# Kernel optimization log

Measured on AMD Instinct MI355X. Metric: run time of the kernel, lower is better.

## Reference

```python
import jax, jax.numpy as jnp
import numpy as np
from jax import lax

B, IMG, P, STRIDE, CIN = 4, 256, 8, 8, 1
D, NH, L = 768, 8, 21
GRID = (IMG - P) // STRIDE + 1  # 32
N = GRID * GRID                 # 1024 tokens
HD = D // NH                    # 96
SCALE = float(HD) ** -0.5


def setup_inputs() -> dict:
    key = jax.random.key(0)
    ks = jax.random.split(key, 9)
    s = 0.02
    return {
        "sam": jax.random.normal(ks[0], (B, CIN, IMG, IMG), dtype=jnp.float32),
        "conv_w": jax.random.normal(ks[1], (D, CIN, P, P), dtype=jnp.float32) * s,
        "conv_b": jnp.zeros((D,), dtype=jnp.float32),
        "ln_g": jnp.ones((D,), dtype=jnp.float32),
        "ln_b": jnp.zeros((D,), dtype=jnp.float32),
        "pos": jax.random.normal(ks[2], (N, D), dtype=jnp.float32) * s,
        "q_w": jax.random.normal(ks[3], (L, D, D), dtype=jnp.float32) * s,
        "kv_w": jax.random.normal(ks[4], (L, D, 2 * D), dtype=jnp.float32) * s,
        "proj_w": jax.random.normal(ks[5], (L, D, D), dtype=jnp.float32) * s,
        "proj_b": jnp.zeros((L, D), dtype=jnp.float32),
    }


def _layernorm(x, g, b, eps=1e-5):
    mu = jnp.mean(x, axis=-1, keepdims=True)
    var = jnp.mean(jnp.square(x - mu), axis=-1, keepdims=True)
    return (x - mu) * lax.rsqrt(var + eps) * g + b


def _guidance(x, qw, kvw, pw, pb):
    b, n, c = x.shape
    q = jnp.einsum('bnc,cd->bnd', x, qw).reshape(b, n, NH, HD).transpose(0, 2, 1, 3)
    kv = jnp.einsum('bnc,cd->bnd', x, kvw)
    k = kv[..., :c].reshape(b, n, NH, HD).transpose(0, 2, 1, 3)
    v = kv[..., c:].reshape(b, n, NH, HD).transpose(0, 2, 1, 3)
    attn = jax.nn.softmax(jnp.einsum('bhnd,bhmd->bhnm', q, k) * SCALE, axis=-1)
    o = jnp.einsum('bhnm,bhmd->bhnd', attn, v).transpose(0, 2, 1, 3).reshape(b, n, c)
    o = jnp.einsum('bnc,cd->bnd', o, pw) + pb
    return o + x  # residual (dropouts are identity in eval)


def reference(sam, conv_w, conv_b, ln_g, ln_b, pos, q_w, kv_w, proj_w, proj_b):
    # Patch embed: conv (valid, stride=patch) -> [B,D,32,32] -> tokens -> LN
    y = lax.conv_general_dilated(sam, conv_w, window_strides=(STRIDE, STRIDE),
                                 padding='VALID',
                                 dimension_numbers=('NCHW', 'OIHW', 'NCHW'))
    y = y + conv_b[None, :, None, None]
    y = y.reshape(B, D, N).transpose(0, 2, 1)  # [B,N,D]
    y = _layernorm(y, ln_g, ln_b)
    x0 = y + pos[None]  # pos_embed(arange) broadcast over batch
    # Faithful to source: each block consumes the SAME x0; output is last block's.
    out = x0
    for i in range(L):
        out = _guidance(x0, q_w[i], kv_w[i], proj_w[i], proj_b[i])
    return out
```

## Files before the change

kernel.cpp:

```cpp
#include <hip/hip_runtime.h>
#include <hip/hip_bf16.h>

typedef __attribute__((ext_vector_type(4))) float f32x4;
typedef __attribute__((ext_vector_type(8))) short s16x8;
typedef unsigned short u16;
typedef unsigned int u32;

#define DEV __device__ __forceinline__

DEV u16 f2bf(float f) {
  union { float f; u32 u; } v; v.f = f;
  u32 r = v.u + 0x7fffu + ((v.u >> 16) & 1u);
  return (u16)(r >> 16);
}

#define MFMA16(a, b, c) __builtin_amdgcn_mfma_f32_16x16x32_bf16((a), (b), (c), 0, 0, 0)
#define GLD16(g, l) __builtin_amdgcn_global_load_lds((const __attribute__((address_space(1))) u32*)(g), (__attribute__((address_space(3))) u32*)(l), 16, 0, 0)

__global__ __launch_bounds__(256) void wcvt_k(const float* __restrict__ src,
                                              u16* __restrict__ dst,
                                              int ncols, float scale) {
  __shared__ float tb[32][33];
  int tile = blockIdx.x;
  int tk = (tile % 24) * 32;
  int tn = (tile / 24) * 32;
  int tx = threadIdx.x & 31, ty = threadIdx.x >> 5;
#pragma unroll
  for (int i = 0; i < 4; i++)
    tb[ty + i * 8][tx] = src[(size_t)(tk + ty + i * 8) * ncols + tn + tx];
  __syncthreads();
#pragma unroll
  for (int i = 0; i < 4; i++)
    dst[(size_t)(tn + ty + i * 8) * 768 + tk + tx] = f2bf(tb[tx][ty + i * 8] * scale);
}

__global__ __launch_bounds__(256) void patch_ln(
    const float* __restrict__ sam, const float* __restrict__ cw,
    const float* __restrict__ cb, const float* __restrict__ g,
    const float* __restrict__ bb, const float* __restrict__ pos,
    float* __restrict__ x0f, u16* __restrict__ x0b) {
  int blk = blockIdx.x;
  int b = blk >> 8, nq = blk & 255;
  int t = threadIdx.x;
  __shared__ float pix[4][64];
  {
    int tk = t >> 6, p = t & 63;
    int n = nq * 4 + tk;
    int gi = n >> 5, gj = n & 31;
    pix[tk][p] = sam[b * 65536 + (gi * 8 + (p >> 3)) * 256 + gj * 8 + (p & 7)];
  }
  __syncthreads();
  float acc[3][4];
#pragma unroll
  for (int u = 0; u < 3; u++) {
    int d = t + u * 256;
    const float4* w4 = (const float4*)(cw + (size_t)d * 64);
    float a0 = cb[d];
    float av0 = a0, av1 = a0, av2 = a0, av3 = a0;
#pragma unroll
    for (int pc = 0; pc < 16; pc++) {
      float4 w = w4[pc];
      av0 += w.x * pix[0][pc * 4] + w.y * pix[0][pc * 4 + 1] + w.z * pix[0][pc * 4 + 2] + w.w * pix[0][pc * 4 + 3];
      av1 += w.x * pix[1][pc * 4] + w.y * pix[1][pc * 4 + 1] + w.z * pix[1][pc * 4 + 2] + w.w * pix[1][pc * 4 + 3];
      av2 += w.x * pix[2][pc * 4] + w.y * pix[2][pc * 4 + 1] + w.z * pix[2][pc * 4 + 2] + w.w * pix[2][pc * 4 + 3];
      av3 += w.x * pix[3][pc * 4] + w.y * pix[3][pc * 4 + 1] + w.z * pix[3][pc * 4 + 2] + w.w * pix[3][pc * 4 + 3];
    }
    acc[u][0] = av0; acc[u][1] = av1; acc[u][2] = av2; acc[u][3] = av3;
  }
  float s1[4], s2[4];
#pragma unroll
  for (int tk = 0; tk < 4; tk++) {
    s1[tk] = acc[0][tk] + acc[1][tk] + acc[2][tk];
    s2[tk] = acc[0][tk] * acc[0][tk] + acc[1][tk] * acc[1][tk] + acc[2][tk] * acc[2][tk];
  }
#pragma unroll
  for (int m = 1; m < 64; m <<= 1) {
#pragma unroll
    for (int tk = 0; tk < 4; tk++) {
      s1[tk] += __shfl_xor(s1[tk], m);
      s2[tk] += __shfl_xor(s2[tk], m);
    }
  }
  __shared__ float red[2][4][4];
  int wid = t >> 6;
  if ((t & 63) == 0) {
#pragma unroll
    for (int tk = 0; tk < 4; tk++) { red[0][wid][tk] = s1[tk]; red[1][wid][tk] = s2[tk]; }
  }
  __syncthreads();
  float mu[4], rs[4];
#pragma unroll
  for (int tk = 0; tk < 4; tk++) {
    float S1 = red[0][0][tk] + red[0][1][tk] + red[0][2][tk] + red[0][3][tk];
    float S2 = red[1][0][tk] + red[1][1][tk] + red[1][2][tk] + red[1][3][tk];
    mu[tk] = S1 * (1.0f / 768.0f);
    float var = S2 * (1.0f / 768.0f) - mu[tk] * mu[tk];
    rs[tk] = rsqrtf(var + 1e-5f);
  }
#pragma unroll
  for (int u = 0; u < 3; u++) {
    int d = t + u * 256;
    float gg = g[d], bbv = bb[d];
#pragma unroll
    for (int tk = 0; tk < 4; tk++) {
      int n = nq * 4 + tk;
      float val = (acc[u][tk] - mu[tk]) * rs[tk] * gg + bbv + pos[(size_t)n * 768 + d];
      size_t idx = ((size_t)(b * 1024 + n)) * 768 + d;
      x0f[idx] = val;
      x0b[idx] = f2bf(val);
    }
  }
}

template <int EPI>
__global__ __launch_bounds__(256, 2) void gemm128(
    const u16* __restrict__ A, const u16* __restrict__ BT, int M, int N, int K,
    u16* __restrict__ q, u16* __restrict__ kk_, u16* __restrict__ vt,
    const float* __restrict__ pb, const float* __restrict__ x0f,
    float* __restrict__ outp) {
  __shared__ __align__(16) u16 Al[128 * 32];
  __shared__ __align__(16) u16 Bl[128 * 32];
  int m0 = blockIdx.y * 128, n0 = blockIdx.x * 128;
  int tid = threadIdx.x, lane = tid & 63, wid = tid >> 6;
  int wr = wid >> 1, wc = wid & 1;
  f32x4 acc[4][4] = {};
  int arow = lane >> 2, acol = (lane & 3) * 8;
  const u16* ag = A + (size_t)(m0 + wid * 32 + arow) * K + acol;
  const u16* bg = BT + (size_t)(n0 + wid * 32 + arow) * K + acol;
  u16* alp = Al + wid * 32 * 32;
  u16* blp = Bl + wid * 32 * 32;
  for (int kt = 0; kt < K; kt += 32) {
    GLD16(ag + kt, alp);
    GLD16(ag + kt + 16 * K, alp + 16 * 32);
    GLD16(bg + kt, blp);
    GLD16(bg + kt + 16 * K, blp + 16 * 32);
    __syncthreads();
    s16x8 af[4], bf[4];
#pragma unroll
    for (int m = 0; m < 4; m++)
      af[m] = *(const s16x8*)&Al[(wr * 64 + m * 16 + (lane & 15)) * 32 + (lane >> 4) * 8];
#pragma unroll
    for (int nn = 0; nn < 4; nn++)
      bf[nn] = *(const s16x8*)&Bl[(wc * 64 + nn * 16 + (lane & 15)) * 32 + (lane >> 4) * 8];
#pragma unroll
    for (int m = 0; m < 4; m++)
#pragma unroll
      for (int nn = 0; nn < 4; nn++)
        acc[m][nn] = MFMA16(af[m], bf[nn], acc[m][nn]);
    __syncthreads();
  }
#pragma unroll
  for (int m = 0; m < 4; m++) {
    int rbase = m0 + wr * 64 + m * 16 + ((lane >> 4) << 2);
#pragma unroll
    for (int nn = 0; nn < 4; nn++) {
      int col = n0 + wc * 64 + nn * 16 + (lane & 15);
      f32x4 v = acc[m][nn];
      if (EPI == 0) {
        if (col < 1536) {
          int cc = (col < 768) ? col : col - 768;
          int h = cc / 96, hd = cc % 96;
          u16* dst = (col < 768) ? q : kk_;
          int bq = (rbase >> 10) * 8 + h;
#pragma unroll
          for (int i = 0; i < 4; i++) {
            int row = rbase + i;
            dst[((size_t)bq * 1024 + (row & 1023)) * 96 + hd] = f2bf(v[i]);
          }
        } else {
          int cc = col - 1536;
          int h = cc / 96, hd = cc % 96;
          int bq = (rbase >> 10) * 8 + h;
          ushort4 pk;
          pk.x = f2bf(v[0]); pk.y = f2bf(v[1]); pk.z = f2bf(v[2]); pk.w = f2bf(v[3]);
          *(ushort4*)&vt[((size_t)bq * 96 + hd) * 1024 + (rbase & 1023)] = pk;
        }
      } else {
        float add = pb[col];
#pragma unroll
        for (int i = 0; i < 4; i++) {
          size_t idx = (size_t)(rbase + i) * 768 + col;
          outp[idx] = v[i] + add + x0f[idx];
        }
      }
    }
  }
}

__global__ __launch_bounds__(256, 2) void attn_k(
    const u16* __restrict__ qg, const u16* __restrict__ kg,
    const u16* __restrict__ vg, u16* __restrict__ o) {
  int bh = blockIdx.x >> 3, qb = blockIdx.x & 7;
  int b = bh >> 3, h = bh & 7;
  int tid = threadIdx.x, lane = tid & 63, wid = tid >> 6;
  int q0 = qb * 128 + wid * 32;
  s16x8 aq[2][3];
#pragma unroll
  for (int mf = 0; mf < 2; mf++)
#pragma unroll
    for (int kc = 0; kc < 3; kc++)
      aq[mf][kc] = *(const s16x8*)&qg[((size_t)bh * 1024 + q0 + mf * 16 + (lane & 15)) * 96 + kc * 32 + (lane >> 4) * 8];
  float mrun[2][4], lrun[2][4];
  f32x4 accO[2][6] = {};
#pragma unroll
  for (int mf = 0; mf < 2; mf++)
#pragma unroll
    for (int i = 0; i < 4; i++) { mrun[mf][i] = -1e30f; lrun[mf][i] = 0.0f; }
  __shared__ __align__(16) u16 Kl[64][104];
  __shared__ __align__(16) u16 VTl[96][72];
  __shared__ __align__(16) u16 Pl[4][32][72];
  const u16* kbase = kg + (size_t)bh * 1024 * 96;
  const u16* vbase = vg + (size_t)bh * 96 * 1024;
  int kkey[3], koff[3], vhd[3], vko[3];
#pragma unroll
  for (int it = 0; it < 3; it++) {
    int c = it * 256 + tid;
    kkey[it] = c / 12; koff[it] = (c % 12) * 8;
    vhd[it] = c >> 3;  vko[it] = (c & 7) * 8;
  }
  for (int kt = 0; kt < 16; kt++) {
#pragma unroll
    for (int it = 0; it < 3; it++) {
      *(uint4*)&Kl[kkey[it]][koff[it]] = *(const uint4*)&kbase[(size_t)(kt * 64 + kkey[it]) * 96 + koff[it]];
      *(uint4*)&VTl[vhd[it]][vko[it]] = *(const uint4*)&vbase[(size_t)vhd[it] * 1024 + kt * 64 + vko[it]];
    }
    __syncthreads();
    f32x4 s[2][4] = {};
#pragma unroll
    for (int nf = 0; nf < 4; nf++) {
#pragma unroll
      for (int kc = 0; kc < 3; kc++) {
        s16x8 bk = *(const s16x8*)&Kl[nf * 16 + (lane & 15)][kc * 32 + (lane >> 4) * 8];
        s[0][nf] = MFMA16(aq[0][kc], bk, s[0][nf]);
        s[1][nf] = MFMA16(aq[1][kc], bk, s[1][nf]);
      }
    }
#pragma unroll
    for (int mf = 0; mf < 2; mf++) {
#pragma unroll
      for (int i = 0; i < 4; i++) {
        float rm = fmaxf(fmaxf(s[mf][0][i], s[mf][1][i]), fmaxf(s[mf][2][i], s[mf][3][i]));
#pragma unroll
        for (int m = 1; m < 16; m <<= 1) rm = fmaxf(rm, __shfl_xor(rm, m));
        float newm = fmaxf(mrun[mf][i], rm);
        float alpha = __expf(mrun[mf][i] - newm);
        float ps = 0.0f;
#pragma unroll
        for (int nf = 0; nf < 4; nf++) {
          float p = __expf(s[mf][nf][i] - newm);
          s[mf][nf][i] = p;
          ps += p;
        }
#pragma unroll
        for (int m = 1; m < 16; m <<= 1) ps += __shfl_xor(ps, m);
        lrun[mf][i] = lrun[mf][i] * alpha + ps;
        mrun[mf][i] = newm;
#pragma unroll
        for (int nf = 0; nf < 6; nf++) accO[mf][nf][i] *= alpha;
      }
#pragma unroll
      for (int nf = 0; nf < 4; nf++)
#pragma unroll
        for (int i = 0; i < 4; i++)
          Pl[wid][mf * 16 + ((lane >> 4) << 2) + i][nf * 16 + (lane & 15)] = f2bf(s[mf][nf][i]);
    }
    asm volatile("s_waitcnt lgkmcnt(0)" ::: "memory");
    __builtin_amdgcn_sched_barrier(0);
#pragma unroll
    for (int kc = 0; kc < 2; kc++) {
      s16x8 ap0 = *(const s16x8*)&Pl[wid][0 + (lane & 15)][kc * 32 + (lane >> 4) * 8];
      s16x8 ap1 = *(const s16x8*)&Pl[wid][16 + (lane & 15)][kc * 32 + (lane >> 4) * 8];
#pragma unroll
      for (int nf = 0; nf < 6; nf++) {
        s16x8 bv = *(const s16x8*)&VTl[nf * 16 + (lane & 15)][kc * 32 + (lane >> 4) * 8];
        accO[0][nf] = MFMA16(ap0, bv, accO[0][nf]);
        accO[1][nf] = MFMA16(ap1, bv, accO[1][nf]);
      }
    }
    __syncthreads();
  }
#pragma unroll
  for (int mf = 0; mf < 2; mf++) {
#pragma unroll
    for (int i = 0; i < 4; i++) {
      float inv = 1.0f / lrun[mf][i];
      int tok = qb * 128 + wid * 32 + mf * 16 + ((lane >> 4) << 2) + i;
      u16* orow = o + ((size_t)(b * 1024 + tok)) * 768 + h * 96;
#pragma unroll
      for (int nf = 0; nf < 6; nf++)
        orow[nf * 16 + (lane & 15)] = f2bf(accO[mf][nf][i] * inv);
    }
  }
}

extern "C" void kernel_launch(void* const* d_in, const int* in_sizes, int n_in,
                              void* d_out, int out_size, void* d_ws, size_t ws_size,
                              hipStream_t stream) {
  const float* sam    = (const float*)d_in[0];
  const float* conv_w = (const float*)d_in[1];
  const float* conv_b = (const float*)d_in[2];
  const float* ln_g   = (const float*)d_in[3];
  const float* ln_b   = (const float*)d_in[4];
  const float* pos    = (const float*)d_in[5];
  const float* q_w    = (const float*)d_in[6] + (size_t)20 * 768 * 768;
  const float* kv_w   = (const float*)d_in[7] + (size_t)20 * 768 * 1536;
  const float* proj_w = (const float*)d_in[8] + (size_t)20 * 768 * 768;
  const float* proj_b = (const float*)d_in[9] + (size_t)20 * 768;

  char* ws = (char*)d_ws;
  float* x0f  = (float*)ws; ws += (size_t)4096 * 768 * 4;
  u16* x0b    = (u16*)ws;   ws += (size_t)4096 * 768 * 2;
  u16* wqkvT  = (u16*)ws;   ws += (size_t)2304 * 768 * 2;
  u16* pwT    = (u16*)ws;   ws += (size_t)768 * 768 * 2;
  u16* qs     = (u16*)ws;   ws += (size_t)32 * 1024 * 96 * 2;
  u16* ks     = (u16*)ws;   ws += (size_t)32 * 1024 * 96 * 2;
  u16* vts    = (u16*)ws;   ws += (size_t)32 * 96 * 1024 * 2;
  u16* ob     = (u16*)ws;   ws += (size_t)4096 * 768 * 2;

  const float SCALE = 0.10206207261596577f;

  wcvt_k<<<24 * 24, 256, 0, stream>>>(q_w, wqkvT, 768, SCALE);
  wcvt_k<<<24 * 48, 256, 0, stream>>>(kv_w, wqkvT + (size_t)768 * 768, 1536, 1.0f);
  wcvt_k<<<24 * 24, 256, 0, stream>>>(proj_w, pwT, 768, 1.0f);
  patch_ln<<<1024, 256, 0, stream>>>(sam, conv_w, conv_b, ln_g, ln_b, pos, x0f, x0b);
  dim3 g1(18, 32);
  gemm128<0><<<g1, 256, 0, stream>>>(x0b, wqkvT, 4096, 2304, 768, qs, ks, vts,
                                     nullptr, nullptr, nullptr);
  attn_k<<<256, 256, 0, stream>>>(qs, ks, vts, ob);
  dim3 g2(6, 32);
  gemm128<1><<<g2, 256, 0, stream>>>(ob, pwT, 4096, 768, 768, nullptr, nullptr,
                                     nullptr, proj_b, x0f, (float*)d_out);
}
```

Before: 337.1 us.

## Merge prep kernels and double-buffer GEMM and attention K/V loads

Merges the three weight-transpose launches and the patch-embed/LayerNorm launch into a single prep kernel, which removes launch overhead and lets those independent jobs run together. The GEMM mainloop now uses two LDS buffers, so the next k-tile's global-to-LDS loads are issued while MFMAs run on the current tile, and one barrier per iteration is dropped. The attention kernel prefetches the next K/V tile into registers during compute and writes them to LDS after the barrier. The cost is double the GEMM LDS footprint and more register pressure in attention, which could reduce occupancy.

```diff
diff --git a/kernel.cpp b/kernel.cpp
--- a/kernel.cpp
+++ b/kernel.cpp
@@ -17,32 +17,45 @@
 #define MFMA16(a, b, c) __builtin_amdgcn_mfma_f32_16x16x32_bf16((a), (b), (c), 0, 0, 0)
 #define GLD16(g, l) __builtin_amdgcn_global_load_lds((const __attribute__((address_space(1))) u32*)(g), (__attribute__((address_space(3))) u32*)(l), 16, 0, 0)
 
-__global__ __launch_bounds__(256) void wcvt_k(const float* __restrict__ src,
-                                              u16* __restrict__ dst,
-                                              int ncols, float scale) {
-  __shared__ float tb[32][33];
-  int tile = blockIdx.x;
-  int tk = (tile % 24) * 32;
-  int tn = (tile / 24) * 32;
-  int tx = threadIdx.x & 31, ty = threadIdx.x >> 5;
-#pragma unroll
-  for (int i = 0; i < 4; i++)
-    tb[ty + i * 8][tx] = src[(size_t)(tk + ty + i * 8) * ncols + tn + tx];
-  __syncthreads();
-#pragma unroll
-  for (int i = 0; i < 4; i++)
-    dst[(size_t)(tn + ty + i * 8) * 768 + tk + tx] = f2bf(tb[tx][ty + i * 8] * scale);
-}
-
-__global__ __launch_bounds__(256) void patch_ln(
+#define QSCALE 0.10206207261596577f
+
+__global__ __launch_bounds__(256) void prep_k(
+    const float* __restrict__ qw, const float* __restrict__ kvw,
+    const float* __restrict__ pw, u16* __restrict__ wqkvT, u16* __restrict__ pwT,
     const float* __restrict__ sam, const float* __restrict__ cw,
     const float* __restrict__ cb, const float* __restrict__ g,
     const float* __restrict__ bb, const float* __restrict__ pos,
     float* __restrict__ x0f, u16* __restrict__ x0b) {
-  int blk = blockIdx.x;
+  __shared__ float tb[32][33];
+  __shared__ float pix[4][64];
+  __shared__ float red[2][4][4];
+  int bid = blockIdx.x;
+  if (bid < 2304) {
+    int ct = bid / 24, kt = (bid % 24) * 32;
+    const float* src;
+    u16* dst;
+    int ncols, tn, dstbase;
+    float scale = 1.0f;
+    if (ct < 24) {
+      src = qw; ncols = 768; tn = ct * 32; dst = wqkvT; dstbase = tn; scale = QSCALE;
+    } else if (ct < 72) {
+      src = kvw; ncols = 1536; tn = (ct - 24) * 32; dst = wqkvT; dstbase = 768 + tn;
+    } else {
+      src = pw; ncols = 768; tn = (ct - 72) * 32; dst = pwT; dstbase = tn;
+    }
+    int tx = threadIdx.x & 31, ty = threadIdx.x >> 5;
+#pragma unroll
+    for (int i = 0; i < 4; i++)
+      tb[ty + i * 8][tx] = src[(size_t)(kt + ty + i * 8) * ncols + tn + tx];
+    __syncthreads();
+#pragma unroll
+    for (int i = 0; i < 4; i++)
+      dst[(size_t)(dstbase + ty + i * 8) * 768 + kt + tx] = f2bf(tb[tx][ty + i * 8] * scale);
+    return;
+  }
+  int blk = bid - 2304;
   int b = blk >> 8, nq = blk & 255;
   int t = threadIdx.x;
-  __shared__ float pix[4][64];
   {
     int tk = t >> 6, p = t & 63;
     int n = nq * 4 + tk;
@@ -81,7 +94,6 @@
       s2[tk] += __shfl_xor(s2[tk], m);
     }
   }
-  __shared__ float red[2][4][4];
   int wid = t >> 6;
   if ((t & 63) == 0) {
 #pragma unroll
@@ -118,8 +130,8 @@
     u16* __restrict__ q, u16* __restrict__ kk_, u16* __restrict__ vt,
     const float* __restrict__ pb, const float* __restrict__ x0f,
     float* __restrict__ outp) {
-  __shared__ __align__(16) u16 Al[128 * 32];
-  __shared__ __align__(16) u16 Bl[128 * 32];
+  __shared__ __align__(16) u16 Al[2][128 * 32];
+  __shared__ __align__(16) u16 Bl[2][128 * 32];
   int m0 = blockIdx.y * 128, n0 = blockIdx.x * 128;
   int tid = threadIdx.x, lane = tid & 63, wid = tid >> 6;
   int wr = wid >> 1, wc = wid & 1;
@@ -127,28 +139,35 @@
   int arow = lane >> 2, acol = (lane & 3) * 8;
   const u16* ag = A + (size_t)(m0 + wid * 32 + arow) * K + acol;
   const u16* bg = BT + (size_t)(n0 + wid * 32 + arow) * K + acol;
-  u16* alp = Al + wid * 32 * 32;
-  u16* blp = Bl + wid * 32 * 32;
-  for (int kt = 0; kt < K; kt += 32) {
-    GLD16(ag + kt, alp);
-    GLD16(ag + kt + 16 * K, alp + 16 * 32);
-    GLD16(bg + kt, blp);
-    GLD16(bg + kt + 16 * K, blp + 16 * 32);
+  int lofs = wid * 32 * 32;
+#define STAGE_G(bufi, kk)                              \
+  do {                                                 \
+    GLD16(ag + (kk), &Al[bufi][lofs]);                 \
+    GLD16(ag + (kk) + 16 * K, &Al[bufi][lofs + 512]);  \
+    GLD16(bg + (kk), &Bl[bufi][lofs]);                 \
+    GLD16(bg + (kk) + 16 * K, &Bl[bufi][lofs + 512]);  \
+  } while (0)
+  STAGE_G(0, 0);
+  int nk = K >> 5;
+  int cur = 0;
+  for (int t = 0; t < nk; t++) {
     __syncthreads();
+    if (t + 1 < nk) STAGE_G(cur ^ 1, (t + 1) * 32);
     s16x8 af[4], bf[4];
 #pragma unroll
     for (int m = 0; m < 4; m++)
-      af[m] = *(const s16x8*)&Al[(wr * 64 + m * 16 + (lane & 15)) * 32 + (lane >> 4) * 8];
+      af[m] = *(const s16x8*)&Al[cur][(wr * 64 + m * 16 + (lane & 15)) * 32 + (lane >> 4) * 8];
 #pragma unroll
     for (int nn = 0; nn < 4; nn++)
-      bf[nn] = *(const s16x8*)&Bl[(wc * 64 + nn * 16 + (lane & 15)) * 32 + (lane >> 4) * 8];
+      bf[nn] = *(const s16x8*)&Bl[cur][(wc * 64 + nn * 16 + (lane & 15)) * 32 + (lane >> 4) * 8];
 #pragma unroll
     for (int m = 0; m < 4; m++)
 #pragma unroll
       for (int nn = 0; nn < 4; nn++)
         acc[m][nn] = MFMA16(af[m], bf[nn], acc[m][nn]);
-    __syncthreads();
-  }
+    cur ^= 1;
+  }
+#undef STAGE_G
 #pragma unroll
   for (int m = 0; m < 4; m++) {
     int rbase = m0 + wr * 64 + m * 16 + ((lane >> 4) << 2);
@@ -218,12 +237,25 @@
     kkey[it] = c / 12; koff[it] = (c % 12) * 8;
     vhd[it] = c >> 3;  vko[it] = (c & 7) * 8;
   }
+  uint4 kreg[3], vreg[3];
+#define ALOAD(kt)                                                                        \
+  do {                                                                                   \
+    _Pragma("unroll") for (int it = 0; it < 3; it++) {                                   \
+      kreg[it] = *(const uint4*)&kbase[(size_t)((kt) * 64 + kkey[it]) * 96 + koff[it]];  \
+      vreg[it] = *(const uint4*)&vbase[(size_t)vhd[it] * 1024 + (kt) * 64 + vko[it]];    \
+    }                                                                                    \
+  } while (0)
+#define AWRITE()                                             \
+  do {                                                       \
+    _Pragma("unroll") for (int it = 0; it < 3; it++) {       \
+      *(uint4*)&Kl[kkey[it]][koff[it]] = kreg[it];           \
+      *(uint4*)&VTl[vhd[it]][vko[it]] = vreg[it];            \
+    }                                                        \
+  } while (0)
+  ALOAD(0);
+  AWRITE();
   for (int kt = 0; kt < 16; kt++) {
-#pragma unroll
-    for (int it = 0; it < 3; it++) {
-      *(uint4*)&Kl[kkey[it]][koff[it]] = *(const uint4*)&kbase[(size_t)(kt * 64 + kkey[it]) * 96 + koff[it]];
-      *(uint4*)&VTl[vhd[it]][vko[it]] = *(const uint4*)&vbase[(size_t)vhd[it] * 1024 + kt * 64 + vko[it]];
-    }
+    if (kt < 15) ALOAD(kt + 1);
     __syncthreads();
     f32x4 s[2][4] = {};
 #pragma unroll
@@ -278,7 +310,10 @@
       }
     }
     __syncthreads();
-  }
+    if (kt < 15) AWRITE();
+  }
+#undef ALOAD
+#undef AWRITE
 #pragma unroll
   for (int mf = 0; mf < 2; mf++) {
 #pragma unroll
@@ -317,12 +352,8 @@
   u16* vts    = (u16*)ws;   ws += (size_t)32 * 96 * 1024 * 2;
   u16* ob     = (u16*)ws;   ws += (size_t)4096 * 768 * 2;
 
-  const float SCALE = 0.10206207261596577f;
-
-  wcvt_k<<<24 * 24, 256, 0, stream>>>(q_w, wqkvT, 768, SCALE);
-  wcvt_k<<<24 * 48, 256, 0, stream>>>(kv_w, wqkvT + (size_t)768 * 768, 1536, 1.0f);
-  wcvt_k<<<24 * 24, 256, 0, stream>>>(proj_w, pwT, 768, 1.0f);
-  patch_ln<<<1024, 256, 0, stream>>>(sam, conv_w, conv_b, ln_g, ln_b, pos, x0f, x0b);
+  prep_k<<<3328, 256, 0, stream>>>(q_w, kv_w, proj_w, wqkvT, pwT, sam, conv_w,
+                                   conv_b, ln_g, ln_b, pos, x0f, x0b);
   dim3 g1(18, 32);
   gemm128<0><<<g1, 256, 0, stream>>>(x0b, wqkvT, 4096, 2304, 768, qs, ks, vts,
                                      nullptr, nullptr, nullptr);
```

Measured after the change: 356.4 us. 5.7% more time.
